# Kernel tuning notes

Measured on AMD Instinct MI355X. Metric: run time of the kernel, lower is better.

Reference implementation:

```python
import jax, jax.numpy as jnp
import numpy as np

H = 512          # hidden_size
B = 1024         # batch
T = 256          # warmup sequence length
NUM_STEPS = 64


def setup_inputs() -> dict:
    key = jax.random.key(0)
    ks = jax.random.split(key, 8)
    bound = 1.0 / np.sqrt(H)  # torch default init for RNN/Linear
    x = jax.random.normal(ks[0], (B, T), dtype=jnp.float32)
    W_ih = jax.random.uniform(ks[1], (H, 1), jnp.float32, -bound, bound)
    W_hh = jax.random.uniform(ks[2], (H, H), jnp.float32, -bound, bound)
    b_ih = jax.random.uniform(ks[3], (H,), jnp.float32, -bound, bound)
    b_hh = jax.random.uniform(ks[4], (H,), jnp.float32, -bound, bound)
    W_fc = jax.random.uniform(ks[5], (1, H), jnp.float32, -bound, bound)
    b_fc = jax.random.uniform(ks[6], (1,), jnp.float32, -bound, bound)
    return {"x": x, "W_ih": W_ih, "W_hh": W_hh, "b_ih": b_ih,
            "b_hh": b_hh, "W_fc": W_fc, "b_fc": b_fc, "num_steps": NUM_STEPS}


def reference(x, W_ih, W_hh, b_ih, b_hh, W_fc, b_fc, num_steps):
    # Phase 1: warmup RNN over the input series. h_t = relu(x_t*W_ih + b_ih + h@W_hh^T + b_hh)
    bias = b_ih + b_hh  # [H]
    w_in = W_ih[:, 0]   # [H], input_size == 1

    def warm_step(h, xt):                      # h: [B,H], xt: [B]
        h = jax.nn.relu(xt[:, None] * w_in[None, :] + h @ W_hh.T + bias)
        return h, None

    h0 = jnp.zeros((B, H), dtype=x.dtype)
    h, _ = jax.lax.scan(warm_step, h0, x.T)    # scan over time: x.T is [T,B]

    def roll_step(h, _):
        y = h @ W_fc.T + b_fc                  # [B,1]
        h = jax.nn.relu(y @ W_ih.T + h @ W_hh.T + bias)
        return h, y

    _, ys = jax.lax.scan(roll_step, h, None, length=num_steps)  # ys: [S,B,1]
    return jnp.transpose(ys, (1, 0, 2))        # [B, num_steps, 1]
```

## Files before the change

kernel.cpp:

```cpp
#include <hip/hip_runtime.h>
#include <stdint.h>

#define H 512
#define B_SZ 1024
#define T_WARM 256
#define NSTEPS 64
#define TOTAL_T (T_WARM + NSTEPS)

#define RPB 16
#define HC 128
#define NTEAM 64
#define NCG 4
#define NBLK 256
#define NTHR 512
#define HSTR 520

typedef __attribute__((ext_vector_type(8))) short bf16x8;
typedef __attribute__((ext_vector_type(4))) float f32x4;

__device__ __forceinline__ ushort f2bf(float f) {
    uint32_t u = __builtin_bit_cast(uint32_t, f);
    u += 0x7FFFu + ((u >> 16) & 1u);
    return (ushort)(u >> 16);
}
__device__ __forceinline__ float bf2f(ushort h) {
    uint32_t u = ((uint32_t)h) << 16;
    return __builtin_bit_cast(float, u);
}

__global__ void prep_kernel(const float* __restrict__ x,
                            const float* __restrict__ W_hh,
                            const float* __restrict__ b_ih,
                            const float* __restrict__ b_hh,
                            ushort* __restrict__ Wh, ushort* __restrict__ Wl,
                            float* __restrict__ bias, float* __restrict__ xT,
                            uint32_t* __restrict__ Hb0, uint32_t* __restrict__ flags) {
    int i = blockIdx.x * NTHR + threadIdx.x;
    Hb0[i] = 0u;
    if (i < 4096) flags[i] = 0u;
    if (i < H * H) {
        float w = W_hh[i];
        ushort hi = f2bf(w);
        float rem = w - bf2f(hi);
        Wh[i] = hi;
        Wl[i] = f2bf(rem);
    }
    if (i < B_SZ * T_WARM) {
        int b = i & (B_SZ - 1), t = i >> 10;
        xT[t * B_SZ + b] = x[b * T_WARM + t];
    }
    if (i < H) bias[i] = b_ih[i] + b_hh[i];
}

__global__ __launch_bounds__(NTHR, 1)
void rnn_kernel(const float* __restrict__ xT,
                const float* __restrict__ W_ih,
                const float* __restrict__ b_fc_p,
                const float* __restrict__ W_fc,
                const ushort* __restrict__ Wh_g,
                const ushort* __restrict__ Wl_g,
                const float* __restrict__ bias_g,
                uint32_t* __restrict__ Hb0, uint32_t* __restrict__ Hb1,
                uint32_t* __restrict__ flags,
                float* __restrict__ out) {
    __shared__ ushort h_hi[2][RPB * HSTR];
    __shared__ ushort h_lo[2][RPB * HSTR];
    __shared__ uint32_t tr[RPB * HC];
    __shared__ float w_fc_s[H];
    __shared__ float w_in_s[HC];
    __shared__ float bias_s[HC];
    __shared__ float sx[RPB];
    __shared__ float sy[RPB];

    const int tid = threadIdx.x;
    const int bid = blockIdx.x;
    const int team = bid & (NTEAM - 1);
    const int cg = bid >> 6;
    const int row0 = team * RPB;
    const int col0 = cg * HC;

    w_fc_s[tid & (H - 1)] = W_fc[tid & (H - 1)];
    if (tid < HC) { w_in_s[tid] = W_ih[col0 + tid]; bias_s[tid] = bias_g[col0 + tid]; }
    const float bfc = b_fc_p[0];

    const int lane = tid & 63;
    const int wv = tid >> 6;
    const int n = lane & 15, q = lane >> 4;

    bf16x8 Bh[16], Bl[16];
    {
        const ushort* wh = Wh_g + (col0 + wv * 16 + n) * H + q * 8;
        const ushort* wl = Wl_g + (col0 + wv * 16 + n) * H + q * 8;
        #pragma unroll
        for (int kt = 0; kt < 16; ++kt) {
            Bh[kt] = *(const bf16x8*)(wh + kt * 32);
            Bl[kt] = *(const bf16x8*)(wl + kt * 32);
        }
    }

    uint32_t* myflag = flags + (team * NCG + cg) * 16;
    const uint32_t* pollflag = flags + (team * NCG + (wv >> 1)) * 16;
    const bool selfw = ((wv >> 1) == cg);

    for (int t = 0; t < TOTAL_T; ++t) {
        float xv = 0.f;
        if (t < T_WARM && tid < RPB) xv = xT[t * B_SZ + row0 + tid];

        uint64_t tmp[8];
        if (t > 0 && selfw) {
            #pragma unroll
            for (int it = 0; it < 8; ++it) {
                int idx = it * 64 + lane;
                int r = idx >> 5, cpair = idx & 31;
                int kloc = (wv & 1) * 64 + cpair * 2;
                const uint32_t* p = &tr[r * HC + kloc];
                tmp[it] = (uint64_t)p[0] | ((uint64_t)p[1] << 32);
            }
        } else {
            if (t > 0) {
                while (__hip_atomic_load(pollflag, __ATOMIC_RELAXED, __HIP_MEMORY_SCOPE_AGENT)
                       < (uint32_t)t)
                    __builtin_amdgcn_s_sleep(1);
            }
            const uint32_t* hb = (t & 1) ? Hb1 : Hb0;
            const uint64_t* src = (const uint64_t*)hb;
            #pragma unroll
            for (int it = 0; it < 8; ++it) {
                int idx = it * 64 + lane;
                int r = idx >> 5, cpair = idx & 31;
                tmp[it] = __hip_atomic_load(src + ((row0 + r) * 256 + wv * 32 + cpair),
                                            __ATOMIC_RELAXED, __HIP_MEMORY_SCOPE_AGENT);
            }
        }

        ushort* hhb = h_hi[t & 1];
        ushort* hlb = h_lo[t & 1];
        #pragma unroll
        for (int it = 0; it < 8; ++it) {
            int idx = it * 64 + lane;
            int r = idx >> 5, cpair = idx & 31;
            int k = wv * 64 + cpair * 2;
            uint64_t u = tmp[it];
            uint32_t w0 = (uint32_t)u, w1 = (uint32_t)(u >> 32);
            uint32_t hw = (w0 >> 16) | (w1 & 0xFFFF0000u);
            uint32_t lw = (w0 & 0xFFFFu) | (w1 << 16);
            *(uint32_t*)(&hhb[r * HSTR + k]) = hw;
            *(uint32_t*)(&hlb[r * HSTR + k]) = lw;
        }
        if (t < T_WARM && tid < RPB) sx[tid] = xv;
        __syncthreads();

        if (t >= T_WARM) {
            if (tid < RPB * 16) {
                int r = tid >> 4, seg = tid & 15;
                const ushort* hh = &hhb[r * HSTR];
                const ushort* hl = &hlb[r * HSTR];
                float s = 0.f;
                #pragma unroll
                for (int kk = 0; kk < 32; ++kk) {
                    int k = seg + kk * 16;
                    s += (bf2f(hh[k]) + bf2f(hl[k])) * w_fc_s[k];
                }
                #pragma unroll
                for (int off = 8; off; off >>= 1) s += __shfl_down(s, off, 16);
                if (seg == 0) {
                    float y = s + bfc;
                    sy[r] = y;
                    if (cg == 0) out[(row0 + r) * NSTEPS + (t - T_WARM)] = y;
                }
            }
            __syncthreads();
        }

        f32x4 acc0 = {0.f, 0.f, 0.f, 0.f}, acc1 = {0.f, 0.f, 0.f, 0.f};
        const ushort* ha = &hhb[n * HSTR] + q * 8;
        const ushort* la = &hlb[n * HSTR] + q * 8;
        #pragma unroll
        for (int kt = 0; kt < 16; kt += 2) {
            {
                bf16x8 ah = *(const bf16x8*)(ha + kt * 32);
                bf16x8 al = *(const bf16x8*)(la + kt * 32);
                acc0 = __builtin_amdgcn_mfma_f32_16x16x32_bf16(ah, Bh[kt], acc0, 0, 0, 0);
                acc0 = __builtin_amdgcn_mfma_f32_16x16x32_bf16(al, Bh[kt], acc0, 0, 0, 0);
                acc0 = __builtin_amdgcn_mfma_f32_16x16x32_bf16(ah, Bl[kt], acc0, 0, 0, 0);
            }
            {
                bf16x8 ah = *(const bf16x8*)(ha + (kt + 1) * 32);
                bf16x8 al = *(const bf16x8*)(la + (kt + 1) * 32);
                acc1 = __builtin_amdgcn_mfma_f32_16x16x32_bf16(ah, Bh[kt + 1], acc1, 0, 0, 0);
                acc1 = __builtin_amdgcn_mfma_f32_16x16x32_bf16(al, Bh[kt + 1], acc1, 0, 0, 0);
                acc1 = __builtin_amdgcn_mfma_f32_16x16x32_bf16(ah, Bl[kt + 1], acc1, 0, 0, 0);
            }
        }

        const int jl = wv * 16 + n;
        const float wi = w_in_s[jl], bj = bias_s[jl];
        uint32_t* dst = ((t & 1) ? Hb0 : Hb1) + col0 + jl;
        #pragma unroll
        for (int i = 0; i < 4; ++i) {
            int m = q * 4 + i;
            float sv = (t < T_WARM) ? sx[m] : sy[m];
            float v = acc0[i] + acc1[i] + sv * wi + bj;
            v = fmaxf(v, 0.f);
            ushort hi = f2bf(v);
            float rem = v - bf2f(hi);
            uint32_t u = ((uint32_t)hi << 16) | (uint32_t)f2bf(rem);
            tr[m * HC + jl] = u;
            __hip_atomic_store(dst + (row0 + m) * H, u, __ATOMIC_RELAXED, __HIP_MEMORY_SCOPE_AGENT);
        }
        __syncthreads();
        if (tid == 0)
            __hip_atomic_store(myflag, (uint32_t)(t + 1), __ATOMIC_RELAXED, __HIP_MEMORY_SCOPE_AGENT);
    }
}

extern "C" void kernel_launch(void* const* d_in, const int* in_sizes, int n_in,
                              void* d_out, int out_size, void* d_ws, size_t ws_size,
                              hipStream_t stream) {
    const float* x    = (const float*)d_in[0];
    const float* W_ih = (const float*)d_in[1];
    const float* W_hh = (const float*)d_in[2];
    const float* b_ih = (const float*)d_in[3];
    const float* b_hh = (const float*)d_in[4];
    const float* W_fc = (const float*)d_in[5];
    const float* b_fc = (const float*)d_in[6];
    float* out = (float*)d_out;

    uint8_t* w = (uint8_t*)d_ws;
    ushort*   Wh    = (ushort*)(w);
    ushort*   Wl    = (ushort*)(w + 524288);
    float*    bias  = (float*)(w + 1048576);
    float*    xT    = (float*)(w + 1052672);
    uint32_t* Hb0   = (uint32_t*)(w + 2101248);
    uint32_t* Hb1   = (uint32_t*)(w + 4198400);
    uint32_t* flags = (uint32_t*)(w + 6295552);

    prep_kernel<<<1024, NTHR, 0, stream>>>(x, W_hh, b_ih, b_hh, Wh, Wl, bias, xT, Hb0, flags);
    rnn_kernel<<<NBLK, NTHR, 0, stream>>>(xT, W_ih, b_fc, W_fc, Wh, Wl, bias, Hb0, Hb1, flags, out);
}
```

Before: 998.9 us.

## Split K across column groups and exchange partial sums instead of hidden state

Each block now owns a 128-wide K slice of the hidden state and computes partial products for all 512 output columns. Partial sums for the peer column groups are sent through global ping-pong message buffers with per-wave point-to-point flags, replacing the full hidden-state broadcast and the single per-block flag. The fc projection is likewise computed as partial dot products and exchanged. The local slice's MFMAs overlap with the wait on peers. This cuts global traffic and barrier points per step, at the cost of more MFMA work per block, more flags to poll, and a changed floating-point summation order.

```diff
diff --git a/kernel.cpp b/kernel.cpp
--- a/kernel.cpp
+++ b/kernel.cpp
@@ -8,24 +8,36 @@
 #define TOTAL_T (T_WARM + NSTEPS)
 
 #define RPB 16
-#define HC 128
 #define NTEAM 64
 #define NCG 4
 #define NBLK 256
 #define NTHR 512
-#define HSTR 520
+#define HSTR 136
+#define MSG_U64 136
+#define MSGS_PER_PING (NTEAM * NCG * 8 * NCG)
+#define PING_U64 ((size_t)MSGS_PER_PING * MSG_U64)
 
 typedef __attribute__((ext_vector_type(8))) short bf16x8;
 typedef __attribute__((ext_vector_type(4))) float f32x4;
 
-__device__ __forceinline__ ushort f2bf(float f) {
+static __device__ __forceinline__ ushort f2bf(float f) {
     uint32_t u = __builtin_bit_cast(uint32_t, f);
     u += 0x7FFFu + ((u >> 16) & 1u);
     return (ushort)(u >> 16);
 }
-__device__ __forceinline__ float bf2f(ushort h) {
+static __device__ __forceinline__ float bf2f(ushort h) {
     uint32_t u = ((uint32_t)h) << 16;
     return __builtin_bit_cast(float, u);
+}
+static __device__ __forceinline__ uint64_t pack2f(float a, float b) {
+    return (uint64_t)__builtin_bit_cast(uint32_t, a) |
+           ((uint64_t)__builtin_bit_cast(uint32_t, b) << 32);
+}
+static __device__ __forceinline__ float lo_f(uint64_t u) {
+    return __builtin_bit_cast(float, (uint32_t)u);
+}
+static __device__ __forceinline__ float hi_f(uint64_t u) {
+    return __builtin_bit_cast(float, (uint32_t)(u >> 32));
 }
 
 __global__ void prep_kernel(const float* __restrict__ x,
@@ -34,16 +46,14 @@
                             const float* __restrict__ b_hh,
                             ushort* __restrict__ Wh, ushort* __restrict__ Wl,
                             float* __restrict__ bias, float* __restrict__ xT,
-                            uint32_t* __restrict__ Hb0, uint32_t* __restrict__ flags) {
+                            uint32_t* __restrict__ flags) {
     int i = blockIdx.x * NTHR + threadIdx.x;
-    Hb0[i] = 0u;
-    if (i < 4096) flags[i] = 0u;
+    if (i < 8192) flags[i] = 0u;
     if (i < H * H) {
         float w = W_hh[i];
         ushort hi = f2bf(w);
-        float rem = w - bf2f(hi);
         Wh[i] = hi;
-        Wl[i] = f2bf(rem);
+        Wl[i] = f2bf(w - bf2f(hi));
     }
     if (i < B_SZ * T_WARM) {
         int b = i & (B_SZ - 1), t = i >> 10;
@@ -52,7 +62,7 @@
     if (i < H) bias[i] = b_ih[i] + b_hh[i];
 }
 
-__global__ __launch_bounds__(NTHR, 1)
+__global__ __launch_bounds__(NTHR, 2)
 void rnn_kernel(const float* __restrict__ xT,
                 const float* __restrict__ W_ih,
                 const float* __restrict__ b_fc_p,
@@ -60,157 +70,197 @@
                 const ushort* __restrict__ Wh_g,
                 const ushort* __restrict__ Wl_g,
                 const float* __restrict__ bias_g,
-                uint32_t* __restrict__ Hb0, uint32_t* __restrict__ Hb1,
+                uint64_t* __restrict__ Pbuf,
                 uint32_t* __restrict__ flags,
                 float* __restrict__ out) {
-    __shared__ ushort h_hi[2][RPB * HSTR];
-    __shared__ ushort h_lo[2][RPB * HSTR];
-    __shared__ uint32_t tr[RPB * HC];
-    __shared__ float w_fc_s[H];
-    __shared__ float w_in_s[HC];
-    __shared__ float bias_s[HC];
-    __shared__ float sx[RPB];
-    __shared__ float sy[RPB];
-
-    const int tid = threadIdx.x;
-    const int bid = blockIdx.x;
+    __shared__ __align__(16) ushort h_hi[2][RPB * HSTR];
+    __shared__ __align__(16) ushort h_lo[2][RPB * HSTR];
+
+    const int tid  = threadIdx.x;
+    const int bid  = blockIdx.x;
     const int team = bid & (NTEAM - 1);
-    const int cg = bid >> 6;
+    const int cg   = bid >> 6;
     const int row0 = team * RPB;
-    const int col0 = cg * HC;
-
-    w_fc_s[tid & (H - 1)] = W_fc[tid & (H - 1)];
-    if (tid < HC) { w_in_s[tid] = W_ih[col0 + tid]; bias_s[tid] = bias_g[col0 + tid]; }
-    const float bfc = b_fc_p[0];
+    const int col0 = cg * 128;
 
     const int lane = tid & 63;
-    const int wv = tid >> 6;
-    const int n = lane & 15, q = lane >> 4;
-
-    bf16x8 Bh[16], Bl[16];
-    {
-        const ushort* wh = Wh_g + (col0 + wv * 16 + n) * H + q * 8;
-        const ushort* wl = Wl_g + (col0 + wv * 16 + n) * H + q * 8;
-        #pragma unroll
-        for (int kt = 0; kt < 16; ++kt) {
-            Bh[kt] = *(const bf16x8*)(wh + kt * 32);
-            Bl[kt] = *(const bf16x8*)(wl + kt * 32);
-        }
-    }
-
-    uint32_t* myflag = flags + (team * NCG + cg) * 16;
-    const uint32_t* pollflag = flags + (team * NCG + (wv >> 1)) * 16;
-    const bool selfw = ((wv >> 1) == cg);
+    const int wv   = tid >> 6;
+    const int n    = lane & 15, q = lane >> 4;
+
+    bf16x8 Bh[4][4], Bl[4][4];
+    #pragma unroll
+    for (int p = 0; p < 4; ++p) {
+        const int jrow = p * 128 + wv * 16 + n;
+        #pragma unroll
+        for (int kt = 0; kt < 4; ++kt) {
+            const int ko = col0 + kt * 32 + q * 8;
+            Bh[p][kt] = *(const bf16x8*)(Wh_g + jrow * H + ko);
+            Bl[p][kt] = *(const bf16x8*)(Wl_g + jrow * H + ko);
+        }
+    }
+    const int jg = col0 + wv * 16 + n;
+    const float w_in = W_ih[jg];
+    const float bj   = bias_g[jg];
+    const float bfc  = b_fc_p[0];
+
+    uint64_t* om[4];
+    const uint64_t* im[4];
+    #pragma unroll
+    for (int p = 0; p < 4; ++p) {
+        om[p] = Pbuf + ((((size_t)team * 4 + p)  * 8 + wv) * 4 + cg) * MSG_U64;
+        im[p] = Pbuf + ((((size_t)team * 4 + cg) * 8 + wv) * 4 + p)  * MSG_U64;
+    }
+    uint32_t* const fst = flags + (((team * 4 + (lane & 3)) * 8 + wv) * 4) + cg;
+    const uint32_t* const fpl = flags + (((team * 4 + cg) * 8 + wv) * 4) + (lane & 3);
+    const bool flane = (lane < 4) && (lane != cg);
+
+    for (int i = tid; i < RPB * HSTR; i += NTHR) { h_hi[0][i] = 0; h_lo[0][i] = 0; }
+    __syncthreads();
 
     for (int t = 0; t < TOTAL_T; ++t) {
-        float xv = 0.f;
-        if (t < T_WARM && tid < RPB) xv = xT[t * B_SZ + row0 + tid];
-
-        uint64_t tmp[8];
-        if (t > 0 && selfw) {
-            #pragma unroll
-            for (int it = 0; it < 8; ++it) {
-                int idx = it * 64 + lane;
-                int r = idx >> 5, cpair = idx & 31;
-                int kloc = (wv & 1) * 64 + cpair * 2;
-                const uint32_t* p = &tr[r * HC + kloc];
-                tmp[it] = (uint64_t)p[0] | ((uint64_t)p[1] << 32);
-            }
+        const int pp = t & 1;
+        const size_t po = pp ? PING_U64 : 0;
+        const bool roll = (t >= T_WARM);
+
+        f32x4 xq = {0.f, 0.f, 0.f, 0.f};
+        if (!roll) xq = *(const f32x4*)(xT + t * B_SZ + row0 + q * 4);
+
+        const ushort* hh = h_hi[pp];
+        const ushort* hl = h_lo[pp];
+        bf16x8 Ah[4], Al[4];
+        #pragma unroll
+        for (int kt = 0; kt < 4; ++kt) {
+            Ah[kt] = *(const bf16x8*)(hh + n * HSTR + kt * 32 + q * 8);
+            Al[kt] = *(const bf16x8*)(hl + n * HSTR + kt * 32 + q * 8);
+        }
+
+        f32x4 acc[4];
+        #pragma unroll
+        for (int p = 0; p < 4; ++p) acc[p] = (f32x4){0.f, 0.f, 0.f, 0.f};
+        #pragma unroll
+        for (int kt = 0; kt < 4; ++kt) {
+            const bf16x8 ah = Ah[kt], al = Al[kt];
+            #pragma unroll
+            for (int p = 0; p < 4; ++p) {
+                if (p != cg) {
+                    acc[p] = __builtin_amdgcn_mfma_f32_16x16x32_bf16(ah, Bh[p][kt], acc[p], 0, 0, 0);
+                    acc[p] = __builtin_amdgcn_mfma_f32_16x16x32_bf16(al, Bh[p][kt], acc[p], 0, 0, 0);
+                    acc[p] = __builtin_amdgcn_mfma_f32_16x16x32_bf16(ah, Bl[p][kt], acc[p], 0, 0, 0);
+                }
+            }
+        }
+        #pragma unroll
+        for (int p = 0; p < 4; ++p) {
+            if (p != cg) {
+                uint64_t* m = om[p] + po;
+                __hip_atomic_store(m + lane * 2,     pack2f(acc[p][0], acc[p][1]),
+                                   __ATOMIC_RELAXED, __HIP_MEMORY_SCOPE_AGENT);
+                __hip_atomic_store(m + lane * 2 + 1, pack2f(acc[p][2], acc[p][3]),
+                                   __ATOMIC_RELAXED, __HIP_MEMORY_SCOPE_AGENT);
+            }
+        }
+
+        float yv = 0.f;
+        if (roll) {
+            #pragma unroll
+            for (int kt = 0; kt < 4; ++kt) {
+                const float* wf = W_fc + col0 + kt * 32 + q * 8;
+                f32x4 w0 = *(const f32x4*)(wf);
+                f32x4 w1 = *(const f32x4*)(wf + 4);
+                #pragma unroll
+                for (int j = 0; j < 4; ++j) {
+                    yv += (bf2f((ushort)Ah[kt][j])     + bf2f((ushort)Al[kt][j]))     * w0[j];
+                    yv += (bf2f((ushort)Ah[kt][j + 4]) + bf2f((ushort)Al[kt][j + 4])) * w1[j];
+                }
+            }
+            yv += __shfl_xor(yv, 16);
+            yv += __shfl_xor(yv, 32);
+            if (lane < 16) {
+                #pragma unroll
+                for (int p = 0; p < 4; ++p) {
+                    if (p != cg) {
+                        uint32_t* yp = (uint32_t*)(om[p] + po + 128);
+                        __hip_atomic_store(yp + lane, __builtin_bit_cast(uint32_t, yv),
+                                           __ATOMIC_RELAXED, __HIP_MEMORY_SCOPE_AGENT);
+                    }
+                }
+            }
+        }
+
+        asm volatile("s_waitcnt vmcnt(0)" ::: "memory");
+        if (flane)
+            __hip_atomic_store(fst, (uint32_t)(t + 1),
+                               __ATOMIC_RELAXED, __HIP_MEMORY_SCOPE_AGENT);
+
+        f32x4 o0 = {0.f, 0.f, 0.f, 0.f}, o1 = {0.f, 0.f, 0.f, 0.f};
+        #pragma unroll
+        for (int p = 0; p < 4; ++p) {
+            if (p == cg) {
+                #pragma unroll
+                for (int kt = 0; kt < 2; ++kt) {
+                    o0 = __builtin_amdgcn_mfma_f32_16x16x32_bf16(Ah[kt],     Bh[p][kt],     o0, 0, 0, 0);
+                    o0 = __builtin_amdgcn_mfma_f32_16x16x32_bf16(Al[kt],     Bh[p][kt],     o0, 0, 0, 0);
+                    o0 = __builtin_amdgcn_mfma_f32_16x16x32_bf16(Ah[kt],     Bl[p][kt],     o0, 0, 0, 0);
+                    o1 = __builtin_amdgcn_mfma_f32_16x16x32_bf16(Ah[kt + 2], Bh[p][kt + 2], o1, 0, 0, 0);
+                    o1 = __builtin_amdgcn_mfma_f32_16x16x32_bf16(Al[kt + 2], Bh[p][kt + 2], o1, 0, 0, 0);
+                    o1 = __builtin_amdgcn_mfma_f32_16x16x32_bf16(Ah[kt + 2], Bl[p][kt + 2], o1, 0, 0, 0);
+                }
+            }
+        }
+
+        {
+            const uint32_t need = (uint32_t)(t + 1);
+            while (true) {
+                uint32_t f = 0xFFFFFFFFu;
+                if (flane)
+                    f = __hip_atomic_load(fpl, __ATOMIC_RELAXED, __HIP_MEMORY_SCOPE_AGENT);
+                if (__all((int)(f >= need))) break;
+                __builtin_amdgcn_s_sleep(1);
+            }
+        }
+
+        f32x4 rsum = {0.f, 0.f, 0.f, 0.f};
+        float ypeer = 0.f;
+        #pragma unroll
+        for (int p = 0; p < 4; ++p) {
+            if (p != cg) {
+                const uint64_t* m = im[p] + po;
+                uint64_t a = __hip_atomic_load(m + lane * 2,     __ATOMIC_RELAXED, __HIP_MEMORY_SCOPE_AGENT);
+                uint64_t b = __hip_atomic_load(m + lane * 2 + 1, __ATOMIC_RELAXED, __HIP_MEMORY_SCOPE_AGENT);
+                rsum[0] += lo_f(a); rsum[1] += hi_f(a);
+                rsum[2] += lo_f(b); rsum[3] += hi_f(b);
+                if (roll) {
+                    uint32_t yw = __hip_atomic_load((const uint32_t*)(m + 128) + n,
+                                                    __ATOMIC_RELAXED, __HIP_MEMORY_SCOPE_AGENT);
+                    ypeer += __builtin_bit_cast(float, yw);
+                }
+            }
+        }
+
+        float sv[4];
+        if (roll) {
+            const float yf = yv + ypeer + bfc;
+            if (cg == 0 && wv == 0 && lane < 16)
+                out[(row0 + lane) * NSTEPS + (t - T_WARM)] = yf;
+            #pragma unroll
+            for (int i = 0; i < 4; ++i) sv[i] = __shfl(yf, q * 4 + i);
         } else {
-            if (t > 0) {
-                while (__hip_atomic_load(pollflag, __ATOMIC_RELAXED, __HIP_MEMORY_SCOPE_AGENT)
-                       < (uint32_t)t)
-                    __builtin_amdgcn_s_sleep(1);
-            }
-            const uint32_t* hb = (t & 1) ? Hb1 : Hb0;
-            const uint64_t* src = (const uint64_t*)hb;
-            #pragma unroll
-            for (int it = 0; it < 8; ++it) {
-                int idx = it * 64 + lane;
-                int r = idx >> 5, cpair = idx & 31;
-                tmp[it] = __hip_atomic_load(src + ((row0 + r) * 256 + wv * 32 + cpair),
-                                            __ATOMIC_RELAXED, __HIP_MEMORY_SCOPE_AGENT);
-            }
-        }
-
-        ushort* hhb = h_hi[t & 1];
-        ushort* hlb = h_lo[t & 1];
-        #pragma unroll
-        for (int it = 0; it < 8; ++it) {
-            int idx = it * 64 + lane;
-            int r = idx >> 5, cpair = idx & 31;
-            int k = wv * 64 + cpair * 2;
-            uint64_t u = tmp[it];
-            uint32_t w0 = (uint32_t)u, w1 = (uint32_t)(u >> 32);
-            uint32_t hw = (w0 >> 16) | (w1 & 0xFFFF0000u);
-            uint32_t lw = (w0 & 0xFFFFu) | (w1 << 16);
-            *(uint32_t*)(&hhb[r * HSTR + k]) = hw;
-            *(uint32_t*)(&hlb[r * HSTR + k]) = lw;
-        }
-        if (t < T_WARM && tid < RPB) sx[tid] = xv;
+            #pragma unroll
+            for (int i = 0; i < 4; ++i) sv[i] = xq[i];
+        }
+        ushort* dh = h_hi[pp ^ 1];
+        ushort* dl = h_lo[pp ^ 1];
+        const int jl = wv * 16 + n;
+        #pragma unroll
+        for (int i = 0; i < 4; ++i) {
+            const int m = q * 4 + i;
+            float v = o0[i] + o1[i] + rsum[i] + sv[i] * w_in + bj;
+            v = fmaxf(v, 0.f);
+            const ushort hb = f2bf(v);
+            dh[m * HSTR + jl] = hb;
+            dl[m * HSTR + jl] = f2bf(v - bf2f(hb));
+        }
         __syncthreads();
-
-        if (t >= T_WARM) {
-            if (tid < RPB * 16) {
-                int r = tid >> 4, seg = tid & 15;
-                const ushort* hh = &hhb[r * HSTR];
-                const ushort* hl = &hlb[r * HSTR];
-                float s = 0.f;
-                #pragma unroll
-                for (int kk = 0; kk < 32; ++kk) {
-                    int k = seg + kk * 16;
-                    s += (bf2f(hh[k]) + bf2f(hl[k])) * w_fc_s[k];
-                }
-                #pragma unroll
-                for (int off = 8; off; off >>= 1) s += __shfl_down(s, off, 16);
-                if (seg == 0) {
-                    float y = s + bfc;
-                    sy[r] = y;
-                    if (cg == 0) out[(row0 + r) * NSTEPS + (t - T_WARM)] = y;
-                }
-            }
-            __syncthreads();
-        }
-
-        f32x4 acc0 = {0.f, 0.f, 0.f, 0.f}, acc1 = {0.f, 0.f, 0.f, 0.f};
-        const ushort* ha = &hhb[n * HSTR] + q * 8;
-        const ushort* la = &hlb[n * HSTR] + q * 8;
-        #pragma unroll
-        for (int kt = 0; kt < 16; kt += 2) {
-            {
-                bf16x8 ah = *(const bf16x8*)(ha + kt * 32);
-                bf16x8 al = *(const bf16x8*)(la + kt * 32);
-                acc0 = __builtin_amdgcn_mfma_f32_16x16x32_bf16(ah, Bh[kt], acc0, 0, 0, 0);
-                acc0 = __builtin_amdgcn_mfma_f32_16x16x32_bf16(al, Bh[kt], acc0, 0, 0, 0);
-                acc0 = __builtin_amdgcn_mfma_f32_16x16x32_bf16(ah, Bl[kt], acc0, 0, 0, 0);
-            }
-            {
-                bf16x8 ah = *(const bf16x8*)(ha + (kt + 1) * 32);
-                bf16x8 al = *(const bf16x8*)(la + (kt + 1) * 32);
-                acc1 = __builtin_amdgcn_mfma_f32_16x16x32_bf16(ah, Bh[kt + 1], acc1, 0, 0, 0);
-                acc1 = __builtin_amdgcn_mfma_f32_16x16x32_bf16(al, Bh[kt + 1], acc1, 0, 0, 0);
-                acc1 = __builtin_amdgcn_mfma_f32_16x16x32_bf16(ah, Bl[kt + 1], acc1, 0, 0, 0);
-            }
-        }
-
-        const int jl = wv * 16 + n;
-        const float wi = w_in_s[jl], bj = bias_s[jl];
-        uint32_t* dst = ((t & 1) ? Hb0 : Hb1) + col0 + jl;
-        #pragma unroll
-        for (int i = 0; i < 4; ++i) {
-            int m = q * 4 + i;
-            float sv = (t < T_WARM) ? sx[m] : sy[m];
-            float v = acc0[i] + acc1[i] + sv * wi + bj;
-            v = fmaxf(v, 0.f);
-            ushort hi = f2bf(v);
-            float rem = v - bf2f(hi);
-            uint32_t u = ((uint32_t)hi << 16) | (uint32_t)f2bf(rem);
-            tr[m * HC + jl] = u;
-            __hip_atomic_store(dst + (row0 + m) * H, u, __ATOMIC_RELAXED, __HIP_MEMORY_SCOPE_AGENT);
-        }
-        __syncthreads();
-        if (tid == 0)
-            __hip_atomic_store(myflag, (uint32_t)(t + 1), __ATOMIC_RELAXED, __HIP_MEMORY_SCOPE_AGENT);
     }
 }
 
@@ -231,10 +281,9 @@
     ushort*   Wl    = (ushort*)(w + 524288);
     float*    bias  = (float*)(w + 1048576);
     float*    xT    = (float*)(w + 1052672);
-    uint32_t* Hb0   = (uint32_t*)(w + 2101248);
-    uint32_t* Hb1   = (uint32_t*)(w + 4198400);
-    uint32_t* flags = (uint32_t*)(w + 6295552);
-
-    prep_kernel<<<1024, NTHR, 0, stream>>>(x, W_hh, b_ih, b_hh, Wh, Wl, bias, xT, Hb0, flags);
-    rnn_kernel<<<NBLK, NTHR, 0, stream>>>(xT, W_ih, b_fc, W_fc, Wh, Wl, bias, Hb0, Hb1, flags, out);
-}
+    uint32_t* flags = (uint32_t*)(w + 2101248);
+    uint64_t* Pbuf  = (uint64_t*)(w + 2134016);
+
+    prep_kernel<<<1024, NTHR, 0, stream>>>(x, W_hh, b_ih, b_hh, Wh, Wl, bias, xT, flags);
+    rnn_kernel<<<NBLK, NTHR, 0, stream>>>(xT, W_ih, b_fc, W_fc, Wh, Wl, bias, Pbuf, flags, out);
+}
```

New measurement: 3.847 ms. 285% more time.

## Split K across wave halves, fuse fc dot into MFMA pass, per-wave flags

Applied to the files above, without the earlier changes.

Waves now split the K dimension in two halves, each computing two 16-column tiles, with a shared-memory reduction between halves. The fc output dot product is computed from the A fragments already loaded in registers, so the separate rollout reduction phase and one barrier go away. Each writer wave publishes its own flag after its stores drain, and consumers poll two flags with one 64-bit load, which replaces the block-wide barrier before signalling. Own-block columns are written straight into the next LDS buffer instead of going through a transfer array. This cuts per-step serialization latency but adds a reduction barrier and more complex flag ordering.

```diff
diff --git a/kernel.cpp b/kernel.cpp
--- a/kernel.cpp
+++ b/kernel.cpp
@@ -8,22 +8,22 @@
 #define TOTAL_T (T_WARM + NSTEPS)
 
 #define RPB 16
-#define HC 128
 #define NTEAM 64
 #define NCG 4
 #define NBLK 256
 #define NTHR 512
-#define HSTR 520
+#define HSTR 536
+#define REDS 20
 
 typedef __attribute__((ext_vector_type(8))) short bf16x8;
 typedef __attribute__((ext_vector_type(4))) float f32x4;
 
-__device__ __forceinline__ ushort f2bf(float f) {
+static __device__ __forceinline__ ushort f2bf(float f) {
     uint32_t u = __builtin_bit_cast(uint32_t, f);
     u += 0x7FFFu + ((u >> 16) & 1u);
     return (ushort)(u >> 16);
 }
-__device__ __forceinline__ float bf2f(ushort h) {
+static __device__ __forceinline__ float bf2f(ushort h) {
     uint32_t u = ((uint32_t)h) << 16;
     return __builtin_bit_cast(float, u);
 }
@@ -41,9 +41,8 @@
     if (i < H * H) {
         float w = W_hh[i];
         ushort hi = f2bf(w);
-        float rem = w - bf2f(hi);
         Wh[i] = hi;
-        Wl[i] = f2bf(rem);
+        Wl[i] = f2bf(w - bf2f(hi));
     }
     if (i < B_SZ * T_WARM) {
         int b = i & (B_SZ - 1), t = i >> 10;
@@ -63,154 +62,197 @@
                 uint32_t* __restrict__ Hb0, uint32_t* __restrict__ Hb1,
                 uint32_t* __restrict__ flags,
                 float* __restrict__ out) {
-    __shared__ ushort h_hi[2][RPB * HSTR];
-    __shared__ ushort h_lo[2][RPB * HSTR];
-    __shared__ uint32_t tr[RPB * HC];
-    __shared__ float w_fc_s[H];
-    __shared__ float w_in_s[HC];
-    __shared__ float bias_s[HC];
-    __shared__ float sx[RPB];
-    __shared__ float sy[RPB];
-
-    const int tid = threadIdx.x;
-    const int bid = blockIdx.x;
+    __shared__ __align__(16) ushort h_hi[2][RPB * HSTR];
+    __shared__ __align__(16) ushort h_lo[2][RPB * HSTR];
+    __shared__ __align__(16) float  red_s[8 * RPB * REDS];
+    __shared__ __align__(16) float  w_fc_s[H];
+    __shared__ float sy2[RPB];
+
+    const int tid  = threadIdx.x;
+    const int bid  = blockIdx.x;
     const int team = bid & (NTEAM - 1);
-    const int cg = bid >> 6;
+    const int cg   = bid >> 6;
     const int row0 = team * RPB;
-    const int col0 = cg * HC;
-
-    w_fc_s[tid & (H - 1)] = W_fc[tid & (H - 1)];
-    if (tid < HC) { w_in_s[tid] = W_ih[col0 + tid]; bias_s[tid] = bias_g[col0 + tid]; }
+    const int col0 = cg * 128;
+
+    const int lane = tid & 63;
+    const int wv   = tid >> 6;
+    const int g    = wv & 3;
+    const int kh   = wv >> 2;
+    const int n    = lane & 15, q = lane >> 4;
+
+    w_fc_s[tid] = W_fc[tid];
+    for (int i = tid; i < RPB * HSTR; i += NTHR) {
+        h_hi[0][i] = 0; h_lo[0][i] = 0;
+        h_hi[1][i] = 0; h_lo[1][i] = 0;
+    }
+
+    bf16x8 Bh[2][8], Bl[2][8];
+    #pragma unroll
+    for (int tt = 0; tt < 2; ++tt) {
+        const int j = col0 + g * 32 + tt * 16 + n;
+        #pragma unroll
+        for (int kt = 0; kt < 8; ++kt) {
+            const int ko = kh * 256 + kt * 32 + q * 8;
+            Bh[tt][kt] = *(const bf16x8*)(Wh_g + j * H + ko);
+            Bl[tt][kt] = *(const bf16x8*)(Wl_g + j * H + ko);
+        }
+    }
+    float wi[2], bj[2];
+    #pragma unroll
+    for (int tt = 0; tt < 2; ++tt) {
+        const int j = col0 + g * 32 + tt * 16 + n;
+        wi[tt] = W_ih[j];
+        bj[tt] = bias_g[j];
+    }
     const float bfc = b_fc_p[0];
 
-    const int lane = tid & 63;
-    const int wv = tid >> 6;
-    const int n = lane & 15, q = lane >> 4;
-
-    bf16x8 Bh[16], Bl[16];
-    {
-        const ushort* wh = Wh_g + (col0 + wv * 16 + n) * H + q * 8;
-        const ushort* wl = Wl_g + (col0 + wv * 16 + n) * H + q * 8;
-        #pragma unroll
-        for (int kt = 0; kt < 16; ++kt) {
-            Bh[kt] = *(const bf16x8*)(wh + kt * 32);
-            Bl[kt] = *(const bf16x8*)(wl + kt * 32);
-        }
-    }
-
-    uint32_t* myflag = flags + (team * NCG + cg) * 16;
-    const uint32_t* pollflag = flags + (team * NCG + (wv >> 1)) * 16;
-    const bool selfw = ((wv >> 1) == cg);
+    const int s = wv;
+    const bool remote = (s >> 1) != cg;
+    const uint64_t* pollp =
+        (const uint64_t*)(flags + (team * 4 + (s >> 1)) * 16 + (s & 1) * 2);
+    uint32_t* const myflag = flags + (team * 4 + cg) * 16 + g;
+
+    __syncthreads();
 
     for (int t = 0; t < TOTAL_T; ++t) {
-        float xv = 0.f;
-        if (t < T_WARM && tid < RPB) xv = xT[t * B_SZ + row0 + tid];
-
-        uint64_t tmp[8];
-        if (t > 0 && selfw) {
+        const int pp = t & 1;
+        const bool roll = (t >= T_WARM);
+
+        f32x4 xq = {0.f, 0.f, 0.f, 0.f};
+        if (!roll && kh == 0)
+            xq = *(const f32x4*)(xT + t * B_SZ + row0 + q * 4);
+
+        if (remote) {
+            if (t > 0) {
+                const uint32_t need = (uint32_t)t;
+                while (true) {
+                    uint64_t f = __hip_atomic_load(pollp, __ATOMIC_RELAXED,
+                                                   __HIP_MEMORY_SCOPE_AGENT);
+                    if ((uint32_t)f >= need && (uint32_t)(f >> 32) >= need) break;
+                    __builtin_amdgcn_s_sleep(1);
+                }
+            }
+            const uint32_t* hb = (t & 1) ? Hb1 : Hb0;
+            const uint64_t* src = (const uint64_t*)hb;
+            uint64_t tmp[8];
             #pragma unroll
             for (int it = 0; it < 8; ++it) {
                 int idx = it * 64 + lane;
-                int r = idx >> 5, cpair = idx & 31;
-                int kloc = (wv & 1) * 64 + cpair * 2;
-                const uint32_t* p = &tr[r * HC + kloc];
-                tmp[it] = (uint64_t)p[0] | ((uint64_t)p[1] << 32);
-            }
-        } else {
-            if (t > 0) {
-                while (__hip_atomic_load(pollflag, __ATOMIC_RELAXED, __HIP_MEMORY_SCOPE_AGENT)
-                       < (uint32_t)t)
-                    __builtin_amdgcn_s_sleep(1);
-            }
-            const uint32_t* hb = (t & 1) ? Hb1 : Hb0;
-            const uint64_t* src = (const uint64_t*)hb;
+                int r = idx >> 5, c = idx & 31;
+                tmp[it] = __hip_atomic_load(src + ((row0 + r) * 256 + s * 32 + c),
+                                            __ATOMIC_RELAXED, __HIP_MEMORY_SCOPE_AGENT);
+            }
+            ushort* hhb = h_hi[pp];
+            ushort* hlb = h_lo[pp];
             #pragma unroll
             for (int it = 0; it < 8; ++it) {
                 int idx = it * 64 + lane;
-                int r = idx >> 5, cpair = idx & 31;
-                tmp[it] = __hip_atomic_load(src + ((row0 + r) * 256 + wv * 32 + cpair),
-                                            __ATOMIC_RELAXED, __HIP_MEMORY_SCOPE_AGENT);
-            }
-        }
-
-        ushort* hhb = h_hi[t & 1];
-        ushort* hlb = h_lo[t & 1];
+                int r = idx >> 5, c = idx & 31;
+                int k = s * 64 + c * 2;
+                uint64_t u = tmp[it];
+                uint32_t w0 = (uint32_t)u, w1 = (uint32_t)(u >> 32);
+                uint32_t hw = (w0 >> 16) | (w1 & 0xFFFF0000u);
+                uint32_t lw = (w0 & 0xFFFFu) | (w1 << 16);
+                *(uint32_t*)(&hhb[r * HSTR + k]) = hw;
+                *(uint32_t*)(&hlb[r * HSTR + k]) = lw;
+            }
+        }
+        __syncthreads();
+
+        const ushort* ha = h_hi[pp] + n * HSTR + kh * 256 + q * 8;
+        const ushort* la = h_lo[pp] + n * HSTR + kh * 256 + q * 8;
+        bf16x8 Ah[8], Al[8];
         #pragma unroll
-        for (int it = 0; it < 8; ++it) {
-            int idx = it * 64 + lane;
-            int r = idx >> 5, cpair = idx & 31;
-            int k = wv * 64 + cpair * 2;
-            uint64_t u = tmp[it];
-            uint32_t w0 = (uint32_t)u, w1 = (uint32_t)(u >> 32);
-            uint32_t hw = (w0 >> 16) | (w1 & 0xFFFF0000u);
-            uint32_t lw = (w0 & 0xFFFFu) | (w1 << 16);
-            *(uint32_t*)(&hhb[r * HSTR + k]) = hw;
-            *(uint32_t*)(&hlb[r * HSTR + k]) = lw;
-        }
-        if (t < T_WARM && tid < RPB) sx[tid] = xv;
+        for (int kt = 0; kt < 8; ++kt) {
+            Ah[kt] = *(const bf16x8*)(ha + kt * 32);
+            Al[kt] = *(const bf16x8*)(la + kt * 32);
+        }
+
+        f32x4 a0 = {0.f, 0.f, 0.f, 0.f}, a1 = {0.f, 0.f, 0.f, 0.f};
+        #pragma unroll
+        for (int kt = 0; kt < 8; ++kt) {
+            const bf16x8 ah = Ah[kt], al = Al[kt];
+            a0 = __builtin_amdgcn_mfma_f32_16x16x32_bf16(ah, Bh[0][kt], a0, 0, 0, 0);
+            a1 = __builtin_amdgcn_mfma_f32_16x16x32_bf16(ah, Bh[1][kt], a1, 0, 0, 0);
+            a0 = __builtin_amdgcn_mfma_f32_16x16x32_bf16(al, Bh[0][kt], a0, 0, 0, 0);
+            a1 = __builtin_amdgcn_mfma_f32_16x16x32_bf16(al, Bh[1][kt], a1, 0, 0, 0);
+            a0 = __builtin_amdgcn_mfma_f32_16x16x32_bf16(ah, Bl[0][kt], a0, 0, 0, 0);
+            a1 = __builtin_amdgcn_mfma_f32_16x16x32_bf16(ah, Bl[1][kt], a1, 0, 0, 0);
+        }
+
+        float yp = 0.f;
+        if (roll) {
+            #pragma unroll
+            for (int kt = 0; kt < 8; ++kt) {
+                const float* wf = &w_fc_s[kh * 256 + kt * 32 + q * 8];
+                f32x4 w0 = *(const f32x4*)wf;
+                f32x4 w1 = *(const f32x4*)(wf + 4);
+                #pragma unroll
+                for (int j = 0; j < 4; ++j) {
+                    yp += (bf2f((ushort)Ah[kt][j])     + bf2f((ushort)Al[kt][j]))     * w0[j];
+                    yp += (bf2f((ushort)Ah[kt][j + 4]) + bf2f((ushort)Al[kt][j + 4])) * w1[j];
+                }
+            }
+            yp += __shfl_xor(yp, 16);
+            yp += __shfl_xor(yp, 32);
+        }
+
+        if (kh == 1) {
+            float* r0 = &red_s[(g * 2 + 0) * RPB * REDS];
+            float* r1 = &red_s[(g * 2 + 1) * RPB * REDS];
+            #pragma unroll
+            for (int i = 0; i < 4; ++i) {
+                const int m = q * 4 + i;
+                r0[m * REDS + n] = a0[i];
+                r1[m * REDS + n] = a1[i];
+            }
+            if (roll && g == 0 && q == 0) sy2[n] = yp;
+        }
         __syncthreads();
 
-        if (t >= T_WARM) {
-            if (tid < RPB * 16) {
-                int r = tid >> 4, seg = tid & 15;
-                const ushort* hh = &hhb[r * HSTR];
-                const ushort* hl = &hlb[r * HSTR];
-                float s = 0.f;
+        if (kh == 0) {
+            const float* r0 = &red_s[(g * 2 + 0) * RPB * REDS];
+            const float* r1 = &red_s[(g * 2 + 1) * RPB * REDS];
+            float yfin = 0.f;
+            if (roll) {
+                yfin = yp + sy2[n] + bfc;
+                if (g == 0 && q == 0)
+                    out[(row0 + n) * NSTEPS + (t - T_WARM)] = yfin;
+            }
+            ushort* dh = h_hi[pp ^ 1];
+            ushort* dl = h_lo[pp ^ 1];
+            uint32_t* hbn = (t & 1) ? Hb0 : Hb1;
+            #pragma unroll
+            for (int i = 0; i < 4; ++i) {
+                const int m = q * 4 + i;
+                const float sv = roll ? __shfl(yfin, m) : xq[i];
                 #pragma unroll
-                for (int kk = 0; kk < 32; ++kk) {
-                    int k = seg + kk * 16;
-                    s += (bf2f(hh[k]) + bf2f(hl[k])) * w_fc_s[k];
+                for (int tt = 0; tt < 2; ++tt) {
+                    const float accv = tt ? a1[i] : a0[i];
+                    const float redv = tt ? r1[m * REDS + n] : r0[m * REDS + n];
+                    float v = accv + redv + sv * wi[tt] + bj[tt];
+                    v = fmaxf(v, 0.f);
+                    const ushort hb16 = f2bf(v);
+                    const ushort lb16 = f2bf(v - bf2f(hb16));
+                    const uint32_t pk = ((uint32_t)hb16 << 16) | lb16;
+                    const int jcol = col0 + g * 32 + tt * 16 + n;
+                    __hip_atomic_store(hbn + (row0 + m) * H + jcol, pk,
+                                       __ATOMIC_RELAXED, __HIP_MEMORY_SCOPE_AGENT);
+                    const uint32_t nb = __shfl_xor(pk, 1);
+                    if ((n & 1) == 0) {
+                        const uint32_t hiw = (pk >> 16)      | (nb & 0xFFFF0000u);
+                        const uint32_t low = (pk & 0xFFFFu)  | (nb << 16);
+                        *(uint32_t*)(&dh[m * HSTR + jcol]) = hiw;
+                        *(uint32_t*)(&dl[m * HSTR + jcol]) = low;
+                    }
                 }
-                #pragma unroll
-                for (int off = 8; off; off >>= 1) s += __shfl_down(s, off, 16);
-                if (seg == 0) {
-                    float y = s + bfc;
-                    sy[r] = y;
-                    if (cg == 0) out[(row0 + r) * NSTEPS + (t - T_WARM)] = y;
-                }
-            }
-            __syncthreads();
-        }
-
-        f32x4 acc0 = {0.f, 0.f, 0.f, 0.f}, acc1 = {0.f, 0.f, 0.f, 0.f};
-        const ushort* ha = &hhb[n * HSTR] + q * 8;
-        const ushort* la = &hlb[n * HSTR] + q * 8;
-        #pragma unroll
-        for (int kt = 0; kt < 16; kt += 2) {
-            {
-                bf16x8 ah = *(const bf16x8*)(ha + kt * 32);
-                bf16x8 al = *(const bf16x8*)(la + kt * 32);
-                acc0 = __builtin_amdgcn_mfma_f32_16x16x32_bf16(ah, Bh[kt], acc0, 0, 0, 0);
-                acc0 = __builtin_amdgcn_mfma_f32_16x16x32_bf16(al, Bh[kt], acc0, 0, 0, 0);
-                acc0 = __builtin_amdgcn_mfma_f32_16x16x32_bf16(ah, Bl[kt], acc0, 0, 0, 0);
-            }
-            {
-                bf16x8 ah = *(const bf16x8*)(ha + (kt + 1) * 32);
-                bf16x8 al = *(const bf16x8*)(la + (kt + 1) * 32);
-                acc1 = __builtin_amdgcn_mfma_f32_16x16x32_bf16(ah, Bh[kt + 1], acc1, 0, 0, 0);
-                acc1 = __builtin_amdgcn_mfma_f32_16x16x32_bf16(al, Bh[kt + 1], acc1, 0, 0, 0);
-                acc1 = __builtin_amdgcn_mfma_f32_16x16x32_bf16(ah, Bl[kt + 1], acc1, 0, 0, 0);
-            }
-        }
-
-        const int jl = wv * 16 + n;
-        const float wi = w_in_s[jl], bj = bias_s[jl];
-        uint32_t* dst = ((t & 1) ? Hb0 : Hb1) + col0 + jl;
-        #pragma unroll
-        for (int i = 0; i < 4; ++i) {
-            int m = q * 4 + i;
-            float sv = (t < T_WARM) ? sx[m] : sy[m];
-            float v = acc0[i] + acc1[i] + sv * wi + bj;
-            v = fmaxf(v, 0.f);
-            ushort hi = f2bf(v);
-            float rem = v - bf2f(hi);
-            uint32_t u = ((uint32_t)hi << 16) | (uint32_t)f2bf(rem);
-            tr[m * HC + jl] = u;
-            __hip_atomic_store(dst + (row0 + m) * H, u, __ATOMIC_RELAXED, __HIP_MEMORY_SCOPE_AGENT);
-        }
-        __syncthreads();
-        if (tid == 0)
-            __hip_atomic_store(myflag, (uint32_t)(t + 1), __ATOMIC_RELAXED, __HIP_MEMORY_SCOPE_AGENT);
+            }
+            asm volatile("s_waitcnt vmcnt(0)" ::: "memory");
+            if (lane == 0)
+                __hip_atomic_store(myflag, (uint32_t)(t + 1),
+                                   __ATOMIC_RELAXED, __HIP_MEMORY_SCOPE_AGENT);
+        }
     }
 }
 
```

Result: slower. 2.058 ms (+106.0%).
